# Kernel optimization log

Measured on AMD Instinct MI355X. Metric: run time of the kernel, lower is better.

Reference implementation:

```python
import jax, jax.numpy as jnp
import numpy as np

NEG = -1e30  # log-space 'zero'


def setup_inputs() -> dict:
    key = jax.random.key(0)
    T, B, C, L = 1000, 32, 2000, 100
    k1, k2 = jax.random.split(key)
    activations = jax.random.normal(k1, (T, B, C), dtype=jnp.float32)
    # targets cannot be blank (blank == 0) -> sample in [1, C)
    targets = jax.random.randint(k2, (B * L,), 1, C, dtype=jnp.int32)
    input_lengths = jnp.full((B,), T, dtype=jnp.int32)
    target_lengths = jnp.full((B,), L, dtype=jnp.int32)
    return {"activations": activations, "targets": targets,
            "input_lengths": input_lengths, "target_lengths": target_lengths}


def _ctc_costs(activations, targets, input_lengths, target_lengths, blank=0):
    """Per-utterance CTC negative log likelihoods via the alpha DP recursion."""
    T, B, C = activations.shape
    L = targets.shape[0] // B  # equal label lengths per utterance (concatenated flat)
    S = 2 * L + 1              # extended label sequence: blank-interleaved
    lp = jax.nn.log_softmax(activations, axis=-1)  # [T,B,C]
    tgt = targets.reshape(B, L)
    ext = jnp.full((B, S), blank, dtype=tgt.dtype).at[:, 1::2].set(tgt)  # [B,S]
    # log-prob of each extended-label symbol at each frame: [T,B,S]
    lp_ext = jnp.take_along_axis(lp, jnp.broadcast_to(ext[None], (T, B, S)), axis=2)
    # skip transition s-2 -> s allowed iff ext[s] != blank and ext[s] != ext[s-2]
    ext_m2 = jnp.concatenate([jnp.full((B, 2), -1, ext.dtype), ext[:, :-2]], axis=1)
    skip = (ext != blank) & (ext != ext_m2)  # [B,S]

    alpha0 = (jnp.full((B, S), NEG, jnp.float32)
              .at[:, 0].set(lp_ext[0, :, 0])
              .at[:, 1].set(lp_ext[0, :, 1]))

    def step(alpha, lp_t):
        a1 = jnp.concatenate([jnp.full((B, 1), NEG, alpha.dtype), alpha[:, :-1]], axis=1)
        a2 = jnp.concatenate([jnp.full((B, 2), NEG, alpha.dtype), alpha[:, :-2]], axis=1)
        a2 = jnp.where(skip, a2, NEG)
        m = jnp.maximum(jnp.maximum(alpha, a1), a2)
        new = m + jnp.log(jnp.exp(alpha - m) + jnp.exp(a1 - m) + jnp.exp(a2 - m)) + lp_t
        return new, new

    _, alphas = jax.lax.scan(step, alpha0, lp_ext[1:])
    alphas = jnp.concatenate([alpha0[None], alphas], axis=0)  # [T,B,S]
    # alpha at the last valid frame of each utterance
    alpha_fin = alphas[input_lengths - 1, jnp.arange(B)]  # [B,S]
    s_last = (2 * target_lengths).astype(jnp.int32)  # final blank position
    a_b = jnp.take_along_axis(alpha_fin, s_last[:, None], axis=1)[:, 0]
    a_l = jnp.take_along_axis(alpha_fin, (s_last - 1)[:, None], axis=1)[:, 0]
    m = jnp.maximum(a_b, a_l)
    return -(m + jnp.log(jnp.exp(a_b - m) + jnp.exp(a_l - m)))  # [B]


def reference(activations, targets, input_lengths, target_lengths):
    # warp-ctc 'mean' reduction: sum(costs) / minibatch / sum(target_lengths)
    costs = _ctc_costs(activations, targets, input_lengths, target_lengths, blank=0)
    B = costs.shape[0]
    return jnp.sum(costs) / B / jnp.sum(target_lengths).astype(jnp.float32)
```

## Files before the change

kernel.cpp:

```cpp
#include <hip/hip_runtime.h>
#include <math.h>


#define BLK 256
#define RING 50
#define AHEAD 48

typedef float f32x4 __attribute__((ext_vector_type(4)));

__global__ __launch_bounds__(BLK) void k_lse_gather(
    const float* __restrict__ act, const int* __restrict__ targets,
    float* __restrict__ p_ext, int T, int B, int C, int L, int S)
{
  int row = blockIdx.x;
  int b = row % B;
  int t = row / B;
  int tid = threadIdx.x;
  const float* rp = act + (size_t)row * (size_t)C;
  const float4* rp4 = (const float4*)rp;
  int C4 = C >> 2;

  float4 x0 = (tid < C4) ? rp4[tid] : make_float4(-3e38f, -3e38f, -3e38f, -3e38f);
  bool h2 = (tid + BLK) < C4;
  float4 x1 = h2 ? rp4[tid + BLK] : make_float4(0.f, 0.f, 0.f, 0.f);
  float m = fmaxf(fmaxf(x0.x, x0.y), fmaxf(x0.z, x0.w));
  if (h2) m = fmaxf(m, fmaxf(fmaxf(x1.x, x1.y), fmaxf(x1.z, x1.w)));
  for (int i = tid + 2 * BLK; i < C4; i += BLK) {
    float4 x = rp4[i];
    m = fmaxf(m, fmaxf(fmaxf(x.x, x.y), fmaxf(x.z, x.w)));
  }
  #pragma unroll
  for (int o = 32; o > 0; o >>= 1) m = fmaxf(m, __shfl_xor(m, o));
  __shared__ float sm[BLK / 64];
  __shared__ float ss[BLK / 64];
  int w = tid >> 6, ln = tid & 63;
  if (ln == 0) sm[w] = m;
  __syncthreads();
  float M = fmaxf(fmaxf(sm[0], sm[1]), fmaxf(sm[2], sm[3]));

  float ssum = 0.f;
  if (tid < C4)
    ssum += expf(x0.x - M) + expf(x0.y - M) + expf(x0.z - M) + expf(x0.w - M);
  if (h2)
    ssum += expf(x1.x - M) + expf(x1.y - M) + expf(x1.z - M) + expf(x1.w - M);
  for (int i = tid + 2 * BLK; i < C4; i += BLK) {
    float4 x = rp4[i];
    ssum += expf(x.x - M) + expf(x.y - M) + expf(x.z - M) + expf(x.w - M);
  }
  #pragma unroll
  for (int o = 32; o > 0; o >>= 1) ssum += __shfl_xor(ssum, o);
  if (ln == 0) ss[w] = ssum;
  __syncthreads();
  float lse = M + logf(ss[0] + ss[1] + ss[2] + ss[3]);

  float* op = p_ext + ((size_t)b * T + t) * 256;
  float p = 0.f;
  if (tid < S) {
    int c = (tid & 1) ? targets[b * L + (tid >> 1)] : 0;
    p = expf(rp[c] - lse);
  }
  op[tid] = p;
}

__device__ __forceinline__ float wave_max64(float x) {
  int t;
  t = __builtin_amdgcn_update_dpp(0, __float_as_int(x), 0x111, 0xF, 0xF, true);
  x = fmaxf(x, __int_as_float(t));
  t = __builtin_amdgcn_update_dpp(0, __float_as_int(x), 0x112, 0xF, 0xF, true);
  x = fmaxf(x, __int_as_float(t));
  t = __builtin_amdgcn_update_dpp(0, __float_as_int(x), 0x114, 0xF, 0xF, true);
  x = fmaxf(x, __int_as_float(t));
  t = __builtin_amdgcn_update_dpp(0, __float_as_int(x), 0x118, 0xF, 0xF, true);
  x = fmaxf(x, __int_as_float(t));
  t = __builtin_amdgcn_update_dpp(0, __float_as_int(x), 0x142, 0xA, 0xF, false);
  x = fmaxf(x, __int_as_float(t));
  t = __builtin_amdgcn_update_dpp(0, __float_as_int(x), 0x143, 0xC, 0xF, false);
  x = fmaxf(x, __int_as_float(t));
  return __int_as_float(__builtin_amdgcn_readlane(__float_as_int(x), 63));
}

__device__ __forceinline__ float shift_up1(float x) {
  int t = __builtin_amdgcn_update_dpp(0, __float_as_int(x), 0x138, 0xF, 0xF, true);
  return __int_as_float(t);
}

__device__ __forceinline__ void gload_lds16(const float* g, float* l) {
  __builtin_amdgcn_global_load_lds(
      (const __attribute__((address_space(1))) void*)(const void*)g,
      (__attribute__((address_space(3))) void*)(void*)l, 16, 0, 0);
}

__global__ __launch_bounds__(64, 1) void k_alpha(
    const float* __restrict__ p_ext, const int* __restrict__ targets,
    const int* __restrict__ ilen, const int* __restrict__ tlen,
    double* __restrict__ costs, int T, int B, int L)
{
  __shared__ float ring[RING * 256];
  __shared__ float sA[260];

  int b = blockIdx.x;
  int l = threadIdx.x;
  int Tb = ilen[b];
  int Lb = tlen[b];
  int S = 2 * Lb + 1;

  const float* pbase = p_ext + (size_t)b * (size_t)T * 256;
  const float4* pb4 = (const float4*)pbase;

  const int* tg = targets + b * L;
  float kf3 = 0.f, kf5 = 0.f, kf7 = 0.f;
  {
    int s;
    s = 4 * l - 1; if (s >= 3 && s < S) { int mm = (s - 1) >> 1; kf3 = (tg[mm] != tg[mm - 1]) ? 1.f : 0.f; }
    s = 4 * l + 1; if (s >= 3 && s < S) { int mm = (s - 1) >> 1; kf5 = (tg[mm] != tg[mm - 1]) ? 1.f : 0.f; }
    s = 4 * l + 3; if (s >= 3 && s < S) { int mm = (s - 1) >> 1; kf7 = (tg[mm] != tg[mm - 1]) ? 1.f : 0.f; }
  }

  const float BIAS = 18446744073709551616.0f;
  float a0 = 0.f, a1 = 0.f, a2 = 0.f, a3 = 0.f;
  {
    float4 p0 = pb4[l];
    if (l == 0) { a0 = p0.x * BIAS; a1 = p0.y * BIAS; }
  }
  int E = -64;

  int NE = (Tb - 1) >> 1;
  int tmax = T - 1;

  for (int r = 1; r <= AHEAD; ++r) {
    int tr = (r > tmax) ? tmax : r;
    gload_lds16(pbase + (size_t)tr * 256 + 4 * l, &ring[(r - 1) * 256]);
  }

  asm volatile("s_waitcnt vmcnt(46)" ::: "memory");
  f32x4 Pb = *(const f32x4*)&ring[0 * 256 + 4 * l];
  f32x4 Pc = *(const f32x4*)&ring[1 * 256 + 4 * l];

  int sr = 2;
  int si = AHEAD;
  for (int e = 0; e < NE; ++e) {
    asm volatile("s_waitcnt vmcnt(44)" ::: "memory");
    f32x4 Nb = *(const f32x4*)&ring[sr * 256 + 4 * l];
    f32x4 Nc = *(const f32x4*)&ring[sr * 256 + 256 + 4 * l];
    {
      int t1 = 49 + 2 * e; if (t1 > tmax) t1 = tmax;
      int t2 = 50 + 2 * e; if (t2 > tmax) t2 = tmax;
      gload_lds16(pbase + (size_t)t1 * 256 + 4 * l, &ring[si * 256]);
      gload_lds16(pbase + (size_t)t2 * 256 + 4 * l, &ring[si * 256 + 256]);
    }
    sr += 2; if (sr >= RING) sr = 0;
    si += 2; if (si >= RING) si = 0;

    float paz = shift_up1(Pb.z), paw = shift_up1(Pb.w);
    float w1 = shift_up1(a1), w2 = shift_up1(a2), w3 = shift_up1(a3);
    float w4 = a0, w5 = a1, w6 = a2, w7 = a3;
    w7 = (w7 + w6 + kf7 * w5) * Pb.w;
    w6 = (w6 + w5) * Pb.z;
    w5 = (w5 + w4 + kf5 * w3) * Pb.y;
    w4 = (w4 + w3) * Pb.x;
    w3 = (w3 + w2 + kf3 * w1) * paw;
    w2 = (w2 + w1) * paz;
    w7 = (w7 + w6 + kf7 * w5) * Pc.w;
    w6 = (w6 + w5) * Pc.z;
    w5 = (w5 + w4 + kf5 * w3) * Pc.y;
    w4 = (w4 + w3) * Pc.x;
    a0 = w4; a1 = w5; a2 = w6; a3 = w7;

    if (e & 1) {
      float mx = fmaxf(fmaxf(a0, a1), fmaxf(a2, a3));
      float Mx = wave_max64(mx);
      int ee = ilogbf(fmaxf(Mx, 1.17549435e-38f)) - 64;
      float sc = ldexpf(1.0f, -ee);
      a0 *= sc; a1 *= sc; a2 *= sc; a3 *= sc;
      E += ee;
    }

    Pb = Nb; Pc = Nc;
  }
  asm volatile("s_waitcnt vmcnt(0)" ::: "memory");

  int t = 1 + 2 * NE;
  if (t < Tb) {
    float4 P = pb4[(size_t)t * 64 + l];
    float u3 = shift_up1(a3);
    float n0 = (a0 + u3) * P.x;
    float n1 = (a1 + a0 + kf5 * u3) * P.y;
    float n2 = (a2 + a1) * P.z;
    float n3 = (a3 + a2 + kf7 * a1) * P.w;
    a0 = n0; a1 = n1; a2 = n2; a3 = n3;
  }

  sA[4 * l + 0] = a0; sA[4 * l + 1] = a1;
  sA[4 * l + 2] = a2; sA[4 * l + 3] = a3;
  __syncthreads();
  if (l == 0) {
    double ab = (double)sA[2 * Lb];
    double al_ = (double)sA[2 * Lb - 1];
    costs[b] = -(log(ab + al_) + (double)E * 0.6931471805599453);
  }
}

__global__ __launch_bounds__(64) void k_final(
    const double* __restrict__ costs, const int* __restrict__ tlen,
    float* __restrict__ out, int B)
{
  int i = threadIdx.x;
  double c = (i < B) ? costs[i] : 0.0;
  double tl = (i < B) ? (double)tlen[i] : 0.0;
  #pragma unroll
  for (int o = 32; o > 0; o >>= 1) {
    c += __shfl_xor(c, o);
    tl += __shfl_xor(tl, o);
  }
  if (i == 0) out[0] = (float)(c / (double)B / tl);
}

extern "C" void kernel_launch(void* const* d_in, const int* in_sizes, int n_in,
                              void* d_out, int out_size, void* d_ws, size_t ws_size,
                              hipStream_t stream) {
  const float* act     = (const float*)d_in[0];
  const int*   targets = (const int*)d_in[1];
  const int*   ilen    = (const int*)d_in[2];
  const int*   tlen    = (const int*)d_in[3];
  float* out = (float*)d_out;

  int B = in_sizes[2];
  int L = in_sizes[1] / B;
  const int T = 1000, C = 2000;
  int S = 2 * L + 1;

  float* p_ext = (float*)d_ws;
  double* costs = (double*)(p_ext + (size_t)B * T * 256);

  k_lse_gather<<<T * B, BLK, 0, stream>>>(act, targets, p_ext, T, B, C, L, S);
  k_alpha<<<B, 64, 0, stream>>>(p_ext, targets, ilen, tlen, costs, T, B, L);
  k_final<<<1, 64, 0, stream>>>(costs, tlen, out, B);
}
```

Measured before the change: 476.5 us.

## Use one wave per row in softmax gather and double-buffered chunked prefetch in alpha

The log-softmax gather kernel now gives each row to a single 64-lane wave, with all 2000 values held in registers and DPP wave reductions, so the block-level shared-memory reductions and barriers go away. The alpha recursion kernel replaces its 48-deep rolling LDS ring and per-step vmcnt waits with two 32-frame chunk buffers that are prefetched in alternation. It waits on all loads only once per chunk. The ilogb/ldexp rescale is swapped for direct exponent-bit manipulation, which cuts the cost of the serial DP step. The risk is a stall at each chunk boundary, because vmcnt(0) there drains the whole prefetch, and the lse kernel now keeps more registers live per thread.

```diff
diff --git a/kernel.cpp b/kernel.cpp
--- a/kernel.cpp
+++ b/kernel.cpp
@@ -3,91 +3,112 @@
 
 
 #define BLK 256
-#define RING 50
-#define AHEAD 48
+#define CH 32
 
 typedef float f32x4 __attribute__((ext_vector_type(4)));
+
+__device__ __forceinline__ float wave_max64(float x) {
+  int t;
+  t = __builtin_amdgcn_update_dpp(0, __float_as_int(x), 0x111, 0xF, 0xF, true);
+  x = fmaxf(x, __int_as_float(t));
+  t = __builtin_amdgcn_update_dpp(0, __float_as_int(x), 0x112, 0xF, 0xF, true);
+  x = fmaxf(x, __int_as_float(t));
+  t = __builtin_amdgcn_update_dpp(0, __float_as_int(x), 0x114, 0xF, 0xF, true);
+  x = fmaxf(x, __int_as_float(t));
+  t = __builtin_amdgcn_update_dpp(0, __float_as_int(x), 0x118, 0xF, 0xF, true);
+  x = fmaxf(x, __int_as_float(t));
+  t = __builtin_amdgcn_update_dpp(0, __float_as_int(x), 0x142, 0xA, 0xF, false);
+  x = fmaxf(x, __int_as_float(t));
+  t = __builtin_amdgcn_update_dpp(0, __float_as_int(x), 0x143, 0xC, 0xF, false);
+  x = fmaxf(x, __int_as_float(t));
+  return __int_as_float(__builtin_amdgcn_readlane(__float_as_int(x), 63));
+}
+
+__device__ __forceinline__ float wave_sum64(float x) {
+  int t;
+  t = __builtin_amdgcn_update_dpp(0, __float_as_int(x), 0x111, 0xF, 0xF, true);
+  x += __int_as_float(t);
+  t = __builtin_amdgcn_update_dpp(0, __float_as_int(x), 0x112, 0xF, 0xF, true);
+  x += __int_as_float(t);
+  t = __builtin_amdgcn_update_dpp(0, __float_as_int(x), 0x114, 0xF, 0xF, true);
+  x += __int_as_float(t);
+  t = __builtin_amdgcn_update_dpp(0, __float_as_int(x), 0x118, 0xF, 0xF, true);
+  x += __int_as_float(t);
+  t = __builtin_amdgcn_update_dpp(0, __float_as_int(x), 0x142, 0xA, 0xF, false);
+  x += __int_as_float(t);
+  t = __builtin_amdgcn_update_dpp(0, __float_as_int(x), 0x143, 0xC, 0xF, false);
+  x += __int_as_float(t);
+  return __int_as_float(__builtin_amdgcn_readlane(__float_as_int(x), 63));
+}
+
+__device__ __forceinline__ float shift_up1(float x) {
+  int t = __builtin_amdgcn_update_dpp(0, __float_as_int(x), 0x138, 0xF, 0xF, true);
+  return __int_as_float(t);
+}
+
+__device__ __forceinline__ void gload_lds16(const float* g, float* l) {
+  __builtin_amdgcn_global_load_lds(
+      (const __attribute__((address_space(1))) void*)(const void*)g,
+      (__attribute__((address_space(3))) void*)(void*)l, 16, 0, 0);
+}
 
 __global__ __launch_bounds__(BLK) void k_lse_gather(
     const float* __restrict__ act, const int* __restrict__ targets,
     float* __restrict__ p_ext, int T, int B, int C, int L, int S)
 {
-  int row = blockIdx.x;
+  int l = threadIdx.x & 63;
+  int row = blockIdx.x * 4 + (threadIdx.x >> 6);
+  if (row >= T * B) return;
   int b = row % B;
   int t = row / B;
-  int tid = threadIdx.x;
   const float* rp = act + (size_t)row * (size_t)C;
   const float4* rp4 = (const float4*)rp;
   int C4 = C >> 2;
 
-  float4 x0 = (tid < C4) ? rp4[tid] : make_float4(-3e38f, -3e38f, -3e38f, -3e38f);
-  bool h2 = (tid + BLK) < C4;
-  float4 x1 = h2 ? rp4[tid + BLK] : make_float4(0.f, 0.f, 0.f, 0.f);
+  const float4 PAD = make_float4(-3e38f, -3e38f, -3e38f, -3e38f);
+  float4 x0 = rp4[l];
+  float4 x1 = rp4[l + 64];
+  float4 x2 = rp4[l + 128];
+  float4 x3 = rp4[l + 192];
+  float4 x4 = rp4[l + 256];
+  float4 x5 = rp4[l + 320];
+  float4 x6 = rp4[l + 384];
+  float4 x7 = (l + 448 < C4) ? rp4[l + 448] : PAD;
+
   float m = fmaxf(fmaxf(x0.x, x0.y), fmaxf(x0.z, x0.w));
-  if (h2) m = fmaxf(m, fmaxf(fmaxf(x1.x, x1.y), fmaxf(x1.z, x1.w)));
-  for (int i = tid + 2 * BLK; i < C4; i += BLK) {
-    float4 x = rp4[i];
-    m = fmaxf(m, fmaxf(fmaxf(x.x, x.y), fmaxf(x.z, x.w)));
-  }
+  m = fmaxf(m, fmaxf(fmaxf(x1.x, x1.y), fmaxf(x1.z, x1.w)));
+  m = fmaxf(m, fmaxf(fmaxf(x2.x, x2.y), fmaxf(x2.z, x2.w)));
+  m = fmaxf(m, fmaxf(fmaxf(x3.x, x3.y), fmaxf(x3.z, x3.w)));
+  m = fmaxf(m, fmaxf(fmaxf(x4.x, x4.y), fmaxf(x4.z, x4.w)));
+  m = fmaxf(m, fmaxf(fmaxf(x5.x, x5.y), fmaxf(x5.z, x5.w)));
+  m = fmaxf(m, fmaxf(fmaxf(x6.x, x6.y), fmaxf(x6.z, x6.w)));
+  m = fmaxf(m, fmaxf(fmaxf(x7.x, x7.y), fmaxf(x7.z, x7.w)));
+  float M = wave_max64(m);
+
+  float s = 0.f;
+  s += expf(x0.x - M) + expf(x0.y - M) + expf(x0.z - M) + expf(x0.w - M);
+  s += expf(x1.x - M) + expf(x1.y - M) + expf(x1.z - M) + expf(x1.w - M);
+  s += expf(x2.x - M) + expf(x2.y - M) + expf(x2.z - M) + expf(x2.w - M);
+  s += expf(x3.x - M) + expf(x3.y - M) + expf(x3.z - M) + expf(x3.w - M);
+  s += expf(x4.x - M) + expf(x4.y - M) + expf(x4.z - M) + expf(x4.w - M);
+  s += expf(x5.x - M) + expf(x5.y - M) + expf(x5.z - M) + expf(x5.w - M);
+  s += expf(x6.x - M) + expf(x6.y - M) + expf(x6.z - M) + expf(x6.w - M);
+  s += expf(x7.x - M) + expf(x7.y - M) + expf(x7.z - M) + expf(x7.w - M);
+  float Ssum = wave_sum64(s);
+  float lse = M + logf(Ssum);
+
+  const int* tg = targets + b * L;
+  float* op = p_ext + ((size_t)b * T + t) * 256;
   #pragma unroll
-  for (int o = 32; o > 0; o >>= 1) m = fmaxf(m, __shfl_xor(m, o));
-  __shared__ float sm[BLK / 64];
-  __shared__ float ss[BLK / 64];
-  int w = tid >> 6, ln = tid & 63;
-  if (ln == 0) sm[w] = m;
-  __syncthreads();
-  float M = fmaxf(fmaxf(sm[0], sm[1]), fmaxf(sm[2], sm[3]));
-
-  float ssum = 0.f;
-  if (tid < C4)
-    ssum += expf(x0.x - M) + expf(x0.y - M) + expf(x0.z - M) + expf(x0.w - M);
-  if (h2)
-    ssum += expf(x1.x - M) + expf(x1.y - M) + expf(x1.z - M) + expf(x1.w - M);
-  for (int i = tid + 2 * BLK; i < C4; i += BLK) {
-    float4 x = rp4[i];
-    ssum += expf(x.x - M) + expf(x.y - M) + expf(x.z - M) + expf(x.w - M);
-  }
-  #pragma unroll
-  for (int o = 32; o > 0; o >>= 1) ssum += __shfl_xor(ssum, o);
-  if (ln == 0) ss[w] = ssum;
-  __syncthreads();
-  float lse = M + logf(ss[0] + ss[1] + ss[2] + ss[3]);
-
-  float* op = p_ext + ((size_t)b * T + t) * 256;
-  float p = 0.f;
-  if (tid < S) {
-    int c = (tid & 1) ? targets[b * L + (tid >> 1)] : 0;
-    p = expf(rp[c] - lse);
-  }
-  op[tid] = p;
-}
-
-__device__ __forceinline__ float wave_max64(float x) {
-  int t;
-  t = __builtin_amdgcn_update_dpp(0, __float_as_int(x), 0x111, 0xF, 0xF, true);
-  x = fmaxf(x, __int_as_float(t));
-  t = __builtin_amdgcn_update_dpp(0, __float_as_int(x), 0x112, 0xF, 0xF, true);
-  x = fmaxf(x, __int_as_float(t));
-  t = __builtin_amdgcn_update_dpp(0, __float_as_int(x), 0x114, 0xF, 0xF, true);
-  x = fmaxf(x, __int_as_float(t));
-  t = __builtin_amdgcn_update_dpp(0, __float_as_int(x), 0x118, 0xF, 0xF, true);
-  x = fmaxf(x, __int_as_float(t));
-  t = __builtin_amdgcn_update_dpp(0, __float_as_int(x), 0x142, 0xA, 0xF, false);
-  x = fmaxf(x, __int_as_float(t));
-  t = __builtin_amdgcn_update_dpp(0, __float_as_int(x), 0x143, 0xC, 0xF, false);
-  x = fmaxf(x, __int_as_float(t));
-  return __int_as_float(__builtin_amdgcn_readlane(__float_as_int(x), 63));
-}
-
-__device__ __forceinline__ float shift_up1(float x) {
-  int t = __builtin_amdgcn_update_dpp(0, __float_as_int(x), 0x138, 0xF, 0xF, true);
-  return __int_as_float(t);
-}
-
-__device__ __forceinline__ void gload_lds16(const float* g, float* l) {
-  __builtin_amdgcn_global_load_lds(
-      (const __attribute__((address_space(1))) void*)(const void*)g,
-      (__attribute__((address_space(3))) void*)(void*)l, 16, 0, 0);
+  for (int q = 0; q < 4; ++q) {
+    int sidx = l + 64 * q;
+    float p = 0.f;
+    if (sidx < S) {
+      int c = (sidx & 1) ? tg[sidx >> 1] : 0;
+      p = expf(rp[c] - lse);
+    }
+    op[sidx] = p;
+  }
 }
 
 __global__ __launch_bounds__(64, 1) void k_alpha(
@@ -95,7 +116,7 @@
     const int* __restrict__ ilen, const int* __restrict__ tlen,
     double* __restrict__ costs, int T, int B, int L)
 {
-  __shared__ float ring[RING * 256];
+  __shared__ float buf[2][CH * 256];
   __shared__ float sA[260];
 
   int b = blockIdx.x;
@@ -106,6 +127,7 @@
 
   const float* pbase = p_ext + (size_t)b * (size_t)T * 256;
   const float4* pb4 = (const float4*)pbase;
+  int tmax = T - 1;
 
   const int* tg = targets + b * L;
   float kf3 = 0.f, kf5 = 0.f, kf7 = 0.f;
@@ -125,57 +147,68 @@
   int E = -64;
 
   int NE = (Tb - 1) >> 1;
-  int tmax = T - 1;
-
-  for (int r = 1; r <= AHEAD; ++r) {
-    int tr = (r > tmax) ? tmax : r;
-    gload_lds16(pbase + (size_t)tr * 256 + 4 * l, &ring[(r - 1) * 256]);
-  }
-
-  asm volatile("s_waitcnt vmcnt(46)" ::: "memory");
-  f32x4 Pb = *(const f32x4*)&ring[0 * 256 + 4 * l];
-  f32x4 Pc = *(const f32x4*)&ring[1 * 256 + 4 * l];
-
-  int sr = 2;
-  int si = AHEAD;
-  for (int e = 0; e < NE; ++e) {
-    asm volatile("s_waitcnt vmcnt(44)" ::: "memory");
-    f32x4 Nb = *(const f32x4*)&ring[sr * 256 + 4 * l];
-    f32x4 Nc = *(const f32x4*)&ring[sr * 256 + 256 + 4 * l];
-    {
-      int t1 = 49 + 2 * e; if (t1 > tmax) t1 = tmax;
-      int t2 = 50 + 2 * e; if (t2 > tmax) t2 = tmax;
-      gload_lds16(pbase + (size_t)t1 * 256 + 4 * l, &ring[si * 256]);
-      gload_lds16(pbase + (size_t)t2 * 256 + 4 * l, &ring[si * 256 + 256]);
+  int NCH = (NE + 15) >> 4;
+
+  #define ISSUE_CHUNK(KK, DST) do {                                          \
+      int _k = (KK);                                                         \
+      _Pragma("unroll")                                                      \
+      for (int _r = 0; _r < CH; ++_r) {                                      \
+        int _t = 1 + CH * _k + _r; if (_t > tmax) _t = tmax;                 \
+        gload_lds16(pbase + (size_t)_t * 256 + 4 * l, (DST) + _r * 256);     \
+      }                                                                      \
+    } while (0)
+
+  ISSUE_CHUNK(0, buf[0]);
+  asm volatile("s_waitcnt vmcnt(0)" ::: "memory");
+  ISSUE_CHUNK(1, buf[1]);
+  f32x4 Pb = *(const f32x4*)&buf[0][0 * 256 + 4 * l];
+  f32x4 Pc = *(const f32x4*)&buf[0][1 * 256 + 4 * l];
+
+  int e = 0;
+  for (int k = 0; k < NCH; ++k) {
+    float* cur = buf[k & 1];
+    float* nxt = buf[(k + 1) & 1];
+    #pragma unroll
+    for (int j = 0; j < 16; ++j) {
+      f32x4 Nb, Nc;
+      if (j < 15) {
+        Nb = *(const f32x4*)&cur[(2 * j + 2) * 256 + 4 * l];
+        Nc = *(const f32x4*)&cur[(2 * j + 3) * 256 + 4 * l];
+      } else {
+        asm volatile("s_waitcnt vmcnt(0)" ::: "memory");
+        ISSUE_CHUNK(k + 2, cur);
+        Nb = *(const f32x4*)&nxt[0 * 256 + 4 * l];
+        Nc = *(const f32x4*)&nxt[1 * 256 + 4 * l];
+      }
+
+      if (e < NE) {
+        float paz = shift_up1(Pb.z), paw = shift_up1(Pb.w);
+        float w1 = shift_up1(a1), w2 = shift_up1(a2), w3 = shift_up1(a3);
+        float w4 = a0, w5 = a1, w6 = a2, w7 = a3;
+        w7 = (w7 + w6 + kf7 * w5) * Pb.w;
+        w6 = (w6 + w5) * Pb.z;
+        w5 = (w5 + w4 + kf5 * w3) * Pb.y;
+        w4 = (w4 + w3) * Pb.x;
+        w3 = (w3 + w2 + kf3 * w1) * paw;
+        w2 = (w2 + w1) * paz;
+        w7 = (w7 + w6 + kf7 * w5) * Pc.w;
+        w6 = (w6 + w5) * Pc.z;
+        w5 = (w5 + w4 + kf5 * w3) * Pc.y;
+        w4 = (w4 + w3) * Pc.x;
+        a0 = w4; a1 = w5; a2 = w6; a3 = w7;
+
+        if (e & 1) {
+          float mx = fmaxf(fmaxf(a0, a1), fmaxf(a2, a3));
+          float Mx = wave_max64(mx);
+          float Mc = fmaxf(Mx, 1.17549435e-38f);
+          int ee = (int)((__float_as_uint(Mc) >> 23) & 0xFFu) - 127 - 64;
+          float sc = __uint_as_float((unsigned)(127 - ee) << 23);
+          a0 *= sc; a1 *= sc; a2 *= sc; a3 *= sc;
+          E += ee;
+        }
+      }
+      Pb = Nb; Pc = Nc; ++e;
     }
-    sr += 2; if (sr >= RING) sr = 0;
-    si += 2; if (si >= RING) si = 0;
-
-    float paz = shift_up1(Pb.z), paw = shift_up1(Pb.w);
-    float w1 = shift_up1(a1), w2 = shift_up1(a2), w3 = shift_up1(a3);
-    float w4 = a0, w5 = a1, w6 = a2, w7 = a3;
-    w7 = (w7 + w6 + kf7 * w5) * Pb.w;
-    w6 = (w6 + w5) * Pb.z;
-    w5 = (w5 + w4 + kf5 * w3) * Pb.y;
-    w4 = (w4 + w3) * Pb.x;
-    w3 = (w3 + w2 + kf3 * w1) * paw;
-    w2 = (w2 + w1) * paz;
-    w7 = (w7 + w6 + kf7 * w5) * Pc.w;
-    w6 = (w6 + w5) * Pc.z;
-    w5 = (w5 + w4 + kf5 * w3) * Pc.y;
-    w4 = (w4 + w3) * Pc.x;
-    a0 = w4; a1 = w5; a2 = w6; a3 = w7;
-
-    if (e & 1) {
-      float mx = fmaxf(fmaxf(a0, a1), fmaxf(a2, a3));
-      float Mx = wave_max64(mx);
-      int ee = ilogbf(fmaxf(Mx, 1.17549435e-38f)) - 64;
-      float sc = ldexpf(1.0f, -ee);
-      a0 *= sc; a1 *= sc; a2 *= sc; a3 *= sc;
-      E += ee;
-    }
-
-    Pb = Nb; Pc = Nc;
   }
   asm volatile("s_waitcnt vmcnt(0)" ::: "memory");
 
@@ -232,7 +265,8 @@
   float* p_ext = (float*)d_ws;
   double* costs = (double*)(p_ext + (size_t)B * T * 256);
 
-  k_lse_gather<<<T * B, BLK, 0, stream>>>(act, targets, p_ext, T, B, C, L, S);
+  int rows = T * B;
+  k_lse_gather<<<(rows + 3) / 4, BLK, 0, stream>>>(act, targets, p_ext, T, B, C, L, S);
   k_alpha<<<B, 64, 0, stream>>>(p_ext, targets, ilen, tlen, costs, T, B, L);
   k_final<<<1, 64, 0, stream>>>(costs, tlen, out, B);
 }
```

After: 440.5 us. 1.08x faster.
